# Optimization experiments

Hardware: AMD Instinct MI355X
Metric: run time of the kernel (lower is better)

The kernel has to match this reference:

```python
import jax, jax.numpy as jnp
import numpy as np

T = 32        # time_step
H = 64        # n_hidden (and dense width)
A = 8         # nb_actions
OBS_DIM = 512
B = 4096      # sequences; obs rows = B*T
LN_EPS = 1e-12  # tf.contrib.layers.layer_norm epsilon


def setup_inputs() -> dict:
    key = jax.random.key(0)
    ks = jax.random.split(key, 10)
    s = 0.1
    return {
        "obs":  jax.random.normal(ks[0], (B * T, OBS_DIM), jnp.float32),
        "W0":   jax.random.normal(ks[1], (OBS_DIM, H), jnp.float32) * s,
        "b0":   jnp.zeros((H,), jnp.float32),
        "gamma": jnp.ones((H,), jnp.float32),
        "beta":  jnp.zeros((H,), jnp.float32),
        "Wfw":  jax.random.normal(ks[2], (2 * H, 4 * H), jnp.float32) * s,
        "bfw":  jnp.zeros((4 * H,), jnp.float32),
        "Wbw":  jax.random.normal(ks[3], (2 * H, 4 * H), jnp.float32) * s,
        "bbw":  jnp.zeros((4 * H,), jnp.float32),
        "Wc":   jax.random.uniform(ks[4], (H, A), jnp.float32, -0.003, 0.003),
        "bc":   jnp.zeros((A,), jnp.float32),
    }


def _lstm_scan(xs, W, b):
    """BasicLSTMCell (forget_bias=1.0). xs: [T, B, H] -> hs: [T, B, H]."""
    nb = xs.shape[1]
    init = (jnp.zeros((nb, H), xs.dtype), jnp.zeros((nb, H), xs.dtype))

    def step(carry, x_t):
        c, h = carry
        z = jnp.concatenate([x_t, h], axis=-1) @ W + b  # [B, 4H]
        i, j, f, o = jnp.split(z, 4, axis=-1)           # TF gate order i,j,f,o
        c = c * jax.nn.sigmoid(f + 1.0) + jax.nn.sigmoid(i) * jnp.tanh(j)
        h = jnp.tanh(c) * jax.nn.sigmoid(o)
        return (c, h), h

    _, hs = jax.lax.scan(step, init, xs)
    return hs


def reference(obs, W0, b0, gamma, beta, Wfw, bfw, Wbw, bbw, Wc, bc):
    # dense(64) + layer_norm + relu
    x = obs @ W0 + b0                                   # [B*T, H]
    mu = jnp.mean(x, axis=-1, keepdims=True)
    var = jnp.mean(jnp.square(x - mu), axis=-1, keepdims=True)
    x = gamma * (x - mu) / jnp.sqrt(var + LN_EPS) + beta
    x = jax.nn.relu(x)

    xt = x.reshape(-1, T, H).transpose(1, 0, 2)          # [T, B, H]
    hs_fw = _lstm_scan(xt, Wfw, bfw)                     # [T, B, H]
    hs_bw = _lstm_scan(xt[::-1], Wbw, bbw)[::-1]         # reverse-in, reverse-out

    # tf.reshape on the (fw, bw) tuple stacks along a new leading axis:
    # [2, B, T, H] -> [2B, T*H, 1]; conv1d(kernel=stride=H) == per-step proj.
    y = jnp.stack([hs_fw.transpose(1, 0, 2), hs_bw.transpose(1, 0, 2)], axis=0)
    y = y.reshape(-1, T, H)                              # [2B, T, H]
    out = jnp.tanh(jnp.einsum('btk,ka->bta', y, Wc) + bc)  # [2B, T, A]
    return out
```

## Files before the change

kernel.cpp:

```cpp
#include <hip/hip_runtime.h>
#include <hip/hip_bf16.h>

typedef __attribute__((ext_vector_type(8))) short bf16x8;
typedef __attribute__((ext_vector_type(4))) float f32x4;

#define MFMA_BF16 __builtin_amdgcn_mfma_f32_16x16x32_bf16

#define GLDS16(gp, lp)                                                        \
  __builtin_amdgcn_global_load_lds(                                           \
      (const __attribute__((address_space(1))) void*)(gp),                    \
      (__attribute__((address_space(3))) void*)(lp), 16, 0, 0)

__device__ __forceinline__ unsigned pk2(float a, float b) {
  __hip_bfloat162 t = __float22bfloat162_rn(make_float2(a, b));
  return *reinterpret_cast<unsigned*>(&t);
}
__device__ __forceinline__ unsigned short f2bf_hw(float f) {
  __hip_bfloat16 h = __float2bfloat16(f);
  return *reinterpret_cast<unsigned short*>(&h);
}
__device__ __forceinline__ float tanh_f(float x) {
  return 1.f - 2.f * __builtin_amdgcn_rcpf(1.f + __expf(2.f * x));
}

__global__ void k0_conv(const float* __restrict__ W0, const float* __restrict__ Wfw,
                        const float* __restrict__ Wbw, unsigned short* __restrict__ wfrag,
                        unsigned short* __restrict__ wlstm) {
  int gid = blockIdx.x * 256 + threadIdx.x;
  if (gid < 4096) {
    int f = gid >> 6, l = gid & 63;
    int k0 = (f >> 2) * 32 + ((l >> 4) << 3);
    int n = (f & 3) * 16 + (l & 15);
    bf16x8 v;
#pragma unroll
    for (int j = 0; j < 8; ++j) v[j] = (short)f2bf_hw(W0[(k0 + j) * 64 + n]);
    *(bf16x8*)(wfrag + gid * 8) = v;
  } else if (gid < 12288) {
    int g2 = gid - 4096;
    const float* W = (g2 < 4096) ? Wfw : Wbw;
    int f = (g2 & 4095) >> 6, l = g2 & 63;
    int wv = f >> 4, gate = (f >> 2) & 3, kf = f & 3;
    int col = gate * 64 + wv * 16 + (l & 15);
    int kr = kf * 32 + ((l >> 4) << 3);
    bf16x8 v;
#pragma unroll
    for (int j = 0; j < 8; ++j) v[j] = (short)f2bf_hw(W[(kr + j) * 256 + col]);
    *(bf16x8*)(wlstm + g2 * 8) = v;
  }
}

__global__ __launch_bounds__(256, 3) void k_dense_ln(
    const float* __restrict__ obs, const unsigned short* __restrict__ wfrag,
    const float* __restrict__ b0, const float* __restrict__ gam,
    const float* __restrict__ bet, unsigned short* __restrict__ xout) {
  __shared__ __align__(16) char lds[49152];
  const int tid = threadIdx.x, w = tid >> 6, l = tid & 63;
  const int g = l >> 4, c = l & 15;
  const long blk64 = (long)blockIdx.x * 64;
  const long rb = blk64 + w * 16;

  float b0v[4], gv[4], bv[4];
#pragma unroll
  for (int nt = 0; nt < 4; ++nt) {
    int col = nt * 16 + c;
    b0v[nt] = b0[col]; gv[nt] = gam[col]; bv[nt] = bet[col];
  }
  const unsigned short* wfl = wfrag + l * 8;
  const char* gB = (const char*)obs + blk64 * 2048;

  const int rlo = w * 4 + g;
  asm volatile("s_waitcnt vmcnt(0)" ::: "memory");

#define K1_STAGE(q)                                                           \
  {                                                                           \
    _Pragma("unroll") for (int i = 0; i < 4; ++i) {                           \
      int row_ = i * 16 + rlo;                                                \
      const char* gp_ = gB + (long)row_ * 2048 + (q) * 256 +                  \
                        (long)((c ^ rlo) * 16);                               \
      char* lp_ = lds + ((q) % 3) * 16384 + (i * 4096 + (w * 64 + l) * 16);   \
      GLDS16(gp_, lp_);                                                       \
    }                                                                         \
  }

  K1_STAGE(0);
  K1_STAGE(1);
  K1_STAGE(2);

  f32x4 acc[4];
#pragma unroll
  for (int nt = 0; nt < 4; ++nt) acc[nt] = (f32x4){0.f, 0.f, 0.f, 0.f};

#pragma unroll
  for (int q = 0; q < 8; ++q) {
    constexpr int VW[8] = {8, 16, 24, 24, 24, 24, 20, 16};
    asm volatile("s_waitcnt vmcnt(%0)" :: "i"(VW[q]) : "memory");
    __builtin_amdgcn_s_barrier();
    __builtin_amdgcn_sched_barrier(0);

    const char* rowb = lds + (q % 3) * 16384 + (w * 16 + c) * 256;
#pragma unroll
    for (int kf = 0; kf < 2; ++kf) {
      int fb = (q * 2 + kf) * 4;
      bf16x8 B0 = *(const bf16x8*)(wfl + (fb + 0) * 512);
      bf16x8 B1 = *(const bf16x8*)(wfl + (fb + 1) * 512);
      bf16x8 B2 = *(const bf16x8*)(wfl + (fb + 2) * 512);
      bf16x8 B3 = *(const bf16x8*)(wfl + (fb + 3) * 512);
      int u0 = kf * 8 + g * 2;
      float4 f0 = *(const float4*)(rowb + ((u0 + 0) ^ c) * 16);
      float4 f1 = *(const float4*)(rowb + ((u0 + 1) ^ c) * 16);
      union { bf16x8 v; unsigned u[4]; } af;
      af.u[0] = pk2(f0.x, f0.y); af.u[1] = pk2(f0.z, f0.w);
      af.u[2] = pk2(f1.x, f1.y); af.u[3] = pk2(f1.z, f1.w);
      acc[0] = MFMA_BF16(af.v, B0, acc[0], 0, 0, 0);
      acc[1] = MFMA_BF16(af.v, B1, acc[1], 0, 0, 0);
      acc[2] = MFMA_BF16(af.v, B2, acc[2], 0, 0, 0);
      acc[3] = MFMA_BF16(af.v, B3, acc[3], 0, 0, 0);
    }
    if (q < 5) {
      __builtin_amdgcn_s_barrier();
      __builtin_amdgcn_sched_barrier(0);
      K1_STAGE(q + 3);
    }
  }

  float vv[4][4], s1[4], s2[4];
#pragma unroll
  for (int r = 0; r < 4; ++r) { s1[r] = 0.f; s2[r] = 0.f; }
#pragma unroll
  for (int nt = 0; nt < 4; ++nt)
#pragma unroll
    for (int r = 0; r < 4; ++r) {
      float val = acc[nt][r] + b0v[nt];
      vv[nt][r] = val; s1[r] += val; s2[r] += val * val;
    }
#pragma unroll
  for (int r = 0; r < 4; ++r) {
#pragma unroll
    for (int m = 1; m <= 8; m <<= 1) {
      s1[r] += __shfl_xor(s1[r], m);
      s2[r] += __shfl_xor(s2[r], m);
    }
  }
  unsigned short* xw = (unsigned short*)lds + w * 1024;
#pragma unroll
  for (int r = 0; r < 4; ++r) {
    float mu = s1[r] * 0.015625f;
    float var = s2[r] * 0.015625f - mu * mu;
    float inv = rsqrtf(var + 1e-12f);
    int row = g * 4 + r;
#pragma unroll
    for (int nt = 0; nt < 4; ++nt) {
      float xn = (vv[nt][r] - mu) * inv * gv[nt] + bv[nt];
      xw[(row * 64 + nt * 16 + c) ^ (g << 3)] = f2bf_hw(fmaxf(xn, 0.f));
    }
  }
#pragma unroll
  for (int m2 = 0; m2 < 2; ++m2) {
    int m = m2 * 64 + l;
    int row = m >> 3, u8 = m & 7;
    bf16x8 v = *(const bf16x8*)(xw + ((row * 64 + u8 * 8) ^ ((row >> 2) << 3)));
    *(bf16x8*)(xout + (rb + row) * 64 + u8 * 8) = v;
  }
}

__global__ __launch_bounds__(256, 2) void k_lstm(
    const unsigned short* __restrict__ x, const unsigned short* __restrict__ wlstm,
    const float* __restrict__ bfw, const float* __restrict__ bbw,
    const float* __restrict__ Wc, const float* __restrict__ bc,
    float* __restrict__ out) {
  __shared__ __align__(16) char xr[8 * 2048];
  __shared__ unsigned short hl[2 * 1024];
  __shared__ float pl[16 * 32 * 8];
  const int tid = threadIdx.x, w = tid >> 6, l = tid & 63;
  const int g = l >> 4, c = l & 15;
  const int dir = blockIdx.x >> 8;
  const int sq = (blockIdx.x & 255) * 16;
  const float* bias = dir ? bbw : bfw;

  bf16x8 Bf[4][4];
  const unsigned short* wl = wlstm + ((long)dir * 4096 + w * 16 * 64) * 8;
#pragma unroll
  for (int gate = 0; gate < 4; ++gate)
#pragma unroll
    for (int kf = 0; kf < 4; ++kf)
      Bf[gate][kf] = *(const bf16x8*)(wl + ((gate * 4 + kf) * 64 + l) * 8);
  float bz[4];
#pragma unroll
  for (int gate = 0; gate < 4; ++gate) bz[gate] = bias[gate * 64 + w * 16 + c];

  bf16x8 Pc[2];
#pragma unroll
  for (int kf = 0; kf < 2; ++kf)
#pragma unroll
    for (int j = 0; j < 8; ++j) Pc[kf][j] = 0;
  float bcv = 0.f;
  if (c < 8) {
#pragma unroll
    for (int kf = 0; kf < 2; ++kf)
#pragma unroll
      for (int j = 0; j < 8; ++j)
        Pc[kf][j] = (short)f2bf_hw(Wc[(kf * 32 + g * 8 + j) * 8 + c]);
    bcv = bc[c];
  }

  asm volatile("s_waitcnt vmcnt(0)" ::: "memory");

  const int ss = l >> 3, sc = l & 7;
#define K2_STAGE(tt)                                                          \
  {                                                                           \
    int te_ = dir ? 31 - (tt) : (tt);                                         \
    _Pragma("unroll") for (int p_ = 0; p_ < 2; ++p_) {                        \
      int s_ = p_ * 8 + ss;                                                   \
      const char* gp_ = (const char*)x +                                      \
          ((long)(sq + s_) * 32 + te_) * 128 + (long)(sc ^ (s_ & 7)) * 16;    \
      char* lp_ = xr + ((tt) & 7) * 2048 + p_ * 1024;                         \
      GLDS16(gp_, lp_);                                                       \
    }                                                                         \
  }

  K2_STAGE(w);
  K2_STAGE(w + 4);

  for (int i = tid; i < 1024; i += 256) ((unsigned*)hl)[i] = 0u;
  float cs[4] = {0.f, 0.f, 0.f, 0.f};

  if (w < 2) asm volatile("s_waitcnt vmcnt(2)" ::: "memory");
  asm volatile("s_waitcnt lgkmcnt(0)" ::: "memory");
  __builtin_amdgcn_s_barrier();
  __builtin_amdgcn_sched_barrier(0);

  const int hq = w >> 1;
  const int hgp = ((w & 1) * 2 + (c >> 3)) * 16;
  const int hlo = c & 7;

  f32x4 accx[4];
  {
    const char* xt = xr + c * 128;
    bf16x8 Ax0 = *(const bf16x8*)(xt + (long)((g) ^ (c & 7)) * 16);
    bf16x8 Ax1 = *(const bf16x8*)(xt + (long)((4 + g) ^ (c & 7)) * 16);
#pragma unroll
    for (int gate = 0; gate < 4; ++gate) {
      f32x4 b = (f32x4){bz[gate], bz[gate], bz[gate], bz[gate]};
      accx[gate] = MFMA_BF16(Ax1, Bf[gate][1],
                             MFMA_BF16(Ax0, Bf[gate][0], b, 0, 0, 0), 0, 0, 0);
    }
  }

  int p = 0;
#pragma unroll 2
  for (int t = 0; t < 32; ++t) {
    bf16x8 Ah0 = *(const bf16x8*)((const char*)hl + p * 2048 + l * 16);
    bf16x8 Ah1 = *(const bf16x8*)((const char*)hl + p * 2048 + 1024 + l * 16);

    f32x4 acc[4];
#pragma unroll
    for (int gate = 0; gate < 4; ++gate)
      acc[gate] = MFMA_BF16(Ah1, Bf[gate][3],
                            MFMA_BF16(Ah0, Bf[gate][2], accx[gate], 0, 0, 0),
                            0, 0, 0);

    if (t + 1 < 32) {
      const char* xt = xr + ((t + 1) & 7) * 2048 + c * 128;
      bf16x8 Ax0 = *(const bf16x8*)(xt + (long)((g) ^ (c & 7)) * 16);
      bf16x8 Ax1 = *(const bf16x8*)(xt + (long)((4 + g) ^ (c & 7)) * 16);
#pragma unroll
      for (int gate = 0; gate < 4; ++gate) {
        f32x4 b = (f32x4){bz[gate], bz[gate], bz[gate], bz[gate]};
        accx[gate] = MFMA_BF16(Ax1, Bf[gate][1],
                               MFMA_BF16(Ax0, Bf[gate][0], b, 0, 0, 0), 0, 0, 0);
      }
    }

    const int wb = (p ^ 1) * 1024;
#pragma unroll
    for (int r = 0; r < 4; ++r) {
      float ei = __expf(-acc[0][r]);
      float ej = __expf(2.f * acc[1][r]);
      float ef = __expf(-(acc[2][r] + 1.f));
      float eo = __expf(-acc[3][r]);
      float p12 = (1.f + ei) * (1.f + ej);
      float r3 = __builtin_amdgcn_rcpf(p12 * (1.f + ef));
      float it = (ej - 1.f) * (1.f + ef) * r3;
      float sf = p12 * r3;
      cs[r] = cs[r] * sf + it;
      float ec = __expf(2.f * cs[r]);
      float r2 = __builtin_amdgcn_rcpf((1.f + eo) * (1.f + ec));
      hl[wb + (hq * 64 + hgp + 4 * g + r) * 8 + hlo] = f2bf_hw((ec - 1.f) * r2);
    }

    if (t + 8 < 32 && w == (t & 3)) K2_STAGE(t + 8);

    if (t + 2 < 32 && w == ((t + 2) & 3))
      asm volatile("s_waitcnt vmcnt(2)" ::: "memory");
    asm volatile("s_waitcnt lgkmcnt(0)" ::: "memory");
    __builtin_amdgcn_s_barrier();
    __builtin_amdgcn_sched_barrier(0);

    if (t >= 1) {
      f32x4 pa = (f32x4){0.f, 0.f, 0.f, 0.f};
      pa = MFMA_BF16(Ah0, Pc[0], pa, 0, 0, 0);
      pa = MFMA_BF16(Ah1, Pc[1], pa, 0, 0, 0);
      if (g == w && c < 8) {
        int tp = dir ? 32 - t : t - 1;
#pragma unroll
        for (int r = 0; r < 4; ++r)
          pl[(4 * g + r) * 256 + tp * 8 + c] = tanh_f(pa[r] + bcv);
      }
    }
    p ^= 1;
  }

  {
    bf16x8 Ph0 = *(const bf16x8*)((const char*)hl + p * 2048 + l * 16);
    bf16x8 Ph1 = *(const bf16x8*)((const char*)hl + p * 2048 + 1024 + l * 16);
    f32x4 pa = (f32x4){0.f, 0.f, 0.f, 0.f};
    pa = MFMA_BF16(Ph0, Pc[0], pa, 0, 0, 0);
    pa = MFMA_BF16(Ph1, Pc[1], pa, 0, 0, 0);
    if (g == w && c < 8) {
      int tp = dir ? 0 : 31;
#pragma unroll
      for (int r = 0; r < 4; ++r)
        pl[(4 * g + r) * 256 + tp * 8 + c] = tanh_f(pa[r] + bcv);
    }
  }

  asm volatile("s_waitcnt lgkmcnt(0)" ::: "memory");
  __builtin_amdgcn_s_barrier();
#pragma unroll
  for (int i = 0; i < 4; ++i) {
    int fi = tid + i * 256;
    int s = fi >> 6, rem = fi & 63;
    int t2 = rem >> 1, a4 = (rem & 1) * 4;
    float4 v = *(const float4*)(pl + s * 256 + t2 * 8 + a4);
    *(float4*)(out + ((long)(dir * 4096 + sq + s) * 32 + t2) * 8 + a4) = v;
  }
}

extern "C" void kernel_launch(void* const* d_in, const int* in_sizes, int n_in,
                              void* d_out, int out_size, void* d_ws, size_t ws_size,
                              hipStream_t stream) {
  const float* obs = (const float*)d_in[0];
  const float* W0  = (const float*)d_in[1];
  const float* b0  = (const float*)d_in[2];
  const float* gam = (const float*)d_in[3];
  const float* bet = (const float*)d_in[4];
  const float* Wfw = (const float*)d_in[5];
  const float* bfw = (const float*)d_in[6];
  const float* Wbw = (const float*)d_in[7];
  const float* bbw = (const float*)d_in[8];
  const float* Wc  = (const float*)d_in[9];
  const float* bc  = (const float*)d_in[10];
  float* out = (float*)d_out;

  unsigned short* wfrag = (unsigned short*)d_ws;
  unsigned short* wlstm = wfrag + 4096 * 8;
  unsigned short* xbf   = wlstm + 8192 * 8;

  k0_conv<<<48, 256, 0, stream>>>(W0, Wfw, Wbw, wfrag, wlstm);
  k_dense_ln<<<2048, 256, 0, stream>>>(obs, wfrag, b0, gam, bet, xbf);
  k_lstm<<<512, 256, 0, stream>>>(xbf, wlstm, bfw, bbw, Wc, bc, out);
}
```

Before: 104.1 us.

## Halve sequences per LSTM block to double grid size and parallelism

```diff
diff --git a/kernel.cpp b/kernel.cpp
--- a/kernel.cpp
+++ b/kernel.cpp
@@ -168,13 +168,13 @@
     const float* __restrict__ bfw, const float* __restrict__ bbw,
     const float* __restrict__ Wc, const float* __restrict__ bc,
     float* __restrict__ out) {
-  __shared__ __align__(16) char xr[8 * 2048];
+  __shared__ __align__(16) char xr[8 * 1024];
   __shared__ unsigned short hl[2 * 1024];
-  __shared__ float pl[16 * 32 * 8];
+  __shared__ float pl[8 * 32 * 8];
   const int tid = threadIdx.x, w = tid >> 6, l = tid & 63;
   const int g = l >> 4, c = l & 15;
-  const int dir = blockIdx.x >> 8;
-  const int sq = (blockIdx.x & 255) * 16;
+  const int dir = blockIdx.x >> 9;
+  const int sq = (blockIdx.x & 511) * 8;
   const float* bias = dir ? bbw : bfw;
 
   bf16x8 Bf[4][4];
@@ -209,13 +209,10 @@
 #define K2_STAGE(tt)                                                          \
   {                                                                           \
     int te_ = dir ? 31 - (tt) : (tt);                                         \
-    _Pragma("unroll") for (int p_ = 0; p_ < 2; ++p_) {                        \
-      int s_ = p_ * 8 + ss;                                                   \
-      const char* gp_ = (const char*)x +                                      \
-          ((long)(sq + s_) * 32 + te_) * 128 + (long)(sc ^ (s_ & 7)) * 16;    \
-      char* lp_ = xr + ((tt) & 7) * 2048 + p_ * 1024;                         \
-      GLDS16(gp_, lp_);                                                       \
-    }                                                                         \
+    const char* gp_ = (const char*)x +                                        \
+        ((long)(sq + ss) * 32 + te_) * 128 + (long)((sc ^ ss) * 16);          \
+    char* lp_ = xr + ((tt) & 7) * 1024;                                       \
+    GLDS16(gp_, lp_);                                                         \
   }
 
   K2_STAGE(w);
@@ -224,20 +221,20 @@
   for (int i = tid; i < 1024; i += 256) ((unsigned*)hl)[i] = 0u;
   float cs[4] = {0.f, 0.f, 0.f, 0.f};
 
-  if (w < 2) asm volatile("s_waitcnt vmcnt(2)" ::: "memory");
+  if (w < 2) asm volatile("s_waitcnt vmcnt(1)" ::: "memory");
   asm volatile("s_waitcnt lgkmcnt(0)" ::: "memory");
   __builtin_amdgcn_s_barrier();
   __builtin_amdgcn_sched_barrier(0);
 
-  const int hq = w >> 1;
-  const int hgp = ((w & 1) * 2 + (c >> 3)) * 16;
-  const int hlo = c & 7;
+  const int hf = w >> 1;
+  const int hlb = 16 * ((w * 2 + (c >> 3)) & 3);
+  const int hj = c & 7;
 
   f32x4 accx[4];
   {
-    const char* xt = xr + c * 128;
-    bf16x8 Ax0 = *(const bf16x8*)(xt + (long)((g) ^ (c & 7)) * 16);
-    bf16x8 Ax1 = *(const bf16x8*)(xt + (long)((4 + g) ^ (c & 7)) * 16);
+    const char* xt = xr + (c & 7) * 128;
+    bf16x8 Ax0 = *(const bf16x8*)(xt + (long)((g ^ (c & 7)) * 16));
+    bf16x8 Ax1 = *(const bf16x8*)(xt + (long)(((4 + g) ^ (c & 7)) * 16));
 #pragma unroll
     for (int gate = 0; gate < 4; ++gate) {
       f32x4 b = (f32x4){bz[gate], bz[gate], bz[gate], bz[gate]};
@@ -260,9 +257,9 @@
                             0, 0, 0);
 
     if (t + 1 < 32) {
-      const char* xt = xr + ((t + 1) & 7) * 2048 + c * 128;
-      bf16x8 Ax0 = *(const bf16x8*)(xt + (long)((g) ^ (c & 7)) * 16);
-      bf16x8 Ax1 = *(const bf16x8*)(xt + (long)((4 + g) ^ (c & 7)) * 16);
+      const char* xt = xr + ((t + 1) & 7) * 1024 + (c & 7) * 128;
+      bf16x8 Ax0 = *(const bf16x8*)(xt + (long)((g ^ (c & 7)) * 16));
+      bf16x8 Ax1 = *(const bf16x8*)(xt + (long)(((4 + g) ^ (c & 7)) * 16));
 #pragma unroll
       for (int gate = 0; gate < 4; ++gate) {
         f32x4 b = (f32x4){bz[gate], bz[gate], bz[gate], bz[gate]};
@@ -272,35 +269,37 @@
     }
 
     const int wb = (p ^ 1) * 1024;
-#pragma unroll
-    for (int r = 0; r < 4; ++r) {
-      float ei = __expf(-acc[0][r]);
-      float ej = __expf(2.f * acc[1][r]);
-      float ef = __expf(-(acc[2][r] + 1.f));
-      float eo = __expf(-acc[3][r]);
-      float p12 = (1.f + ei) * (1.f + ej);
-      float r3 = __builtin_amdgcn_rcpf(p12 * (1.f + ef));
-      float it = (ej - 1.f) * (1.f + ef) * r3;
-      float sf = p12 * r3;
-      cs[r] = cs[r] * sf + it;
-      float ec = __expf(2.f * cs[r]);
-      float r2 = __builtin_amdgcn_rcpf((1.f + eo) * (1.f + ec));
-      hl[wb + (hq * 64 + hgp + 4 * g + r) * 8 + hlo] = f2bf_hw((ec - 1.f) * r2);
-    }
-
-    if (t + 8 < 32 && w == (t & 3)) K2_STAGE(t + 8);
+    if (g < 2) {
+#pragma unroll
+      for (int r = 0; r < 4; ++r) {
+        float ei = __expf(-acc[0][r]);
+        float ej = __expf(2.f * acc[1][r]);
+        float ef = __expf(-(acc[2][r] + 1.f));
+        float eo = __expf(-acc[3][r]);
+        float p12 = (1.f + ei) * (1.f + ej);
+        float r3 = __builtin_amdgcn_rcpf(p12 * (1.f + ef));
+        float it = (ej - 1.f) * (1.f + ef) * r3;
+        float sf = p12 * r3;
+        cs[r] = cs[r] * sf + it;
+        float ec = __expf(2.f * cs[r]);
+        float r2 = __builtin_amdgcn_rcpf((1.f + eo) * (1.f + ec));
+        hl[wb + hf * 512 + (hlb + 4 * g + r) * 8 + hj] = f2bf_hw((ec - 1.f) * r2);
+      }
+    }
 
     if (t + 2 < 32 && w == ((t + 2) & 3))
-      asm volatile("s_waitcnt vmcnt(2)" ::: "memory");
+      asm volatile("s_waitcnt vmcnt(1)" ::: "memory");
     asm volatile("s_waitcnt lgkmcnt(0)" ::: "memory");
     __builtin_amdgcn_s_barrier();
     __builtin_amdgcn_sched_barrier(0);
+
+    if (t + 8 < 32 && w == (t & 3)) K2_STAGE(t + 8);
 
     if (t >= 1) {
       f32x4 pa = (f32x4){0.f, 0.f, 0.f, 0.f};
       pa = MFMA_BF16(Ah0, Pc[0], pa, 0, 0, 0);
       pa = MFMA_BF16(Ah1, Pc[1], pa, 0, 0, 0);
-      if (g == w && c < 8) {
+      if (w < 2 && g == w && c < 8) {
         int tp = dir ? 32 - t : t - 1;
 #pragma unroll
         for (int r = 0; r < 4; ++r)
@@ -316,7 +315,7 @@
     f32x4 pa = (f32x4){0.f, 0.f, 0.f, 0.f};
     pa = MFMA_BF16(Ph0, Pc[0], pa, 0, 0, 0);
     pa = MFMA_BF16(Ph1, Pc[1], pa, 0, 0, 0);
-    if (g == w && c < 8) {
+    if (w < 2 && g == w && c < 8) {
       int tp = dir ? 0 : 31;
 #pragma unroll
       for (int r = 0; r < 4; ++r)
@@ -327,7 +326,7 @@
   asm volatile("s_waitcnt lgkmcnt(0)" ::: "memory");
   __builtin_amdgcn_s_barrier();
 #pragma unroll
-  for (int i = 0; i < 4; ++i) {
+  for (int i = 0; i < 2; ++i) {
     int fi = tid + i * 256;
     int s = fi >> 6, rem = fi & 63;
     int t2 = rem >> 1, a4 = (rem & 1) * 4;
@@ -358,5 +357,5 @@
 
   k0_conv<<<48, 256, 0, stream>>>(W0, Wfw, Wbw, wfrag, wlstm);
   k_dense_ln<<<2048, 256, 0, stream>>>(obs, wfrag, b0, gam, bet, xbf);
-  k_lstm<<<512, 256, 0, stream>>>(xbf, wlstm, bfw, bbw, Wc, bc, out);
-}
+  k_lstm<<<1024, 256, 0, stream>>>(xbf, wlstm, bfw, bbw, Wc, bc, out);
+}
```

Result: slower. 127.6 us (+22.5%).

## Replace LDS-staged obs pipeline with direct register prefetch in dense+LN kernel

Applied to the files above, without the earlier changes.

```diff
diff --git a/kernel.cpp b/kernel.cpp
--- a/kernel.cpp
+++ b/kernel.cpp
@@ -53,11 +53,10 @@
     const float* __restrict__ obs, const unsigned short* __restrict__ wfrag,
     const float* __restrict__ b0, const float* __restrict__ gam,
     const float* __restrict__ bet, unsigned short* __restrict__ xout) {
-  __shared__ __align__(16) char lds[49152];
+  __shared__ unsigned short xs[4096];
   const int tid = threadIdx.x, w = tid >> 6, l = tid & 63;
   const int g = l >> 4, c = l & 15;
-  const long blk64 = (long)blockIdx.x * 64;
-  const long rb = blk64 + w * 16;
+  const long rb = (long)blockIdx.x * 64 + w * 16;
 
   float b0v[4], gv[4], bv[4];
 #pragma unroll
@@ -65,61 +64,49 @@
     int col = nt * 16 + c;
     b0v[nt] = b0[col]; gv[nt] = gam[col]; bv[nt] = bet[col];
   }
+
+  const float* arow = obs + (rb + c) * 512 + g * 8;
   const unsigned short* wfl = wfrag + l * 8;
-  const char* gB = (const char*)obs + blk64 * 2048;
-
-  const int rlo = w * 4 + g;
-  asm volatile("s_waitcnt vmcnt(0)" ::: "memory");
-
-#define K1_STAGE(q)                                                           \
-  {                                                                           \
-    _Pragma("unroll") for (int i = 0; i < 4; ++i) {                           \
-      int row_ = i * 16 + rlo;                                                \
-      const char* gp_ = gB + (long)row_ * 2048 + (q) * 256 +                  \
-                        (long)((c ^ rlo) * 16);                               \
-      char* lp_ = lds + ((q) % 3) * 16384 + (i * 4096 + (w * 64 + l) * 16);   \
-      GLDS16(gp_, lp_);                                                       \
-    }                                                                         \
-  }
-
-  K1_STAGE(0);
-  K1_STAGE(1);
-  K1_STAGE(2);
+
+  float4 pa[4], pb[4];
+#pragma unroll
+  for (int d = 0; d < 4; ++d) {
+    pa[d] = *(const float4*)(arow + d * 32);
+    pb[d] = *(const float4*)(arow + d * 32 + 4);
+  }
+  bf16x8 Bc[4];
+#pragma unroll
+  for (int nt = 0; nt < 4; ++nt) Bc[nt] = *(const bf16x8*)(wfl + nt * 512);
 
   f32x4 acc[4];
 #pragma unroll
   for (int nt = 0; nt < 4; ++nt) acc[nt] = (f32x4){0.f, 0.f, 0.f, 0.f};
 
 #pragma unroll
-  for (int q = 0; q < 8; ++q) {
-    constexpr int VW[8] = {8, 16, 24, 24, 24, 24, 20, 16};
-    asm volatile("s_waitcnt vmcnt(%0)" :: "i"(VW[q]) : "memory");
-    __builtin_amdgcn_s_barrier();
-    __builtin_amdgcn_sched_barrier(0);
-
-    const char* rowb = lds + (q % 3) * 16384 + (w * 16 + c) * 256;
-#pragma unroll
-    for (int kf = 0; kf < 2; ++kf) {
-      int fb = (q * 2 + kf) * 4;
-      bf16x8 B0 = *(const bf16x8*)(wfl + (fb + 0) * 512);
-      bf16x8 B1 = *(const bf16x8*)(wfl + (fb + 1) * 512);
-      bf16x8 B2 = *(const bf16x8*)(wfl + (fb + 2) * 512);
-      bf16x8 B3 = *(const bf16x8*)(wfl + (fb + 3) * 512);
-      int u0 = kf * 8 + g * 2;
-      float4 f0 = *(const float4*)(rowb + ((u0 + 0) ^ c) * 16);
-      float4 f1 = *(const float4*)(rowb + ((u0 + 1) ^ c) * 16);
-      union { bf16x8 v; unsigned u[4]; } af;
-      af.u[0] = pk2(f0.x, f0.y); af.u[1] = pk2(f0.z, f0.w);
-      af.u[2] = pk2(f1.x, f1.y); af.u[3] = pk2(f1.z, f1.w);
-      acc[0] = MFMA_BF16(af.v, B0, acc[0], 0, 0, 0);
-      acc[1] = MFMA_BF16(af.v, B1, acc[1], 0, 0, 0);
-      acc[2] = MFMA_BF16(af.v, B2, acc[2], 0, 0, 0);
-      acc[3] = MFMA_BF16(af.v, B3, acc[3], 0, 0, 0);
-    }
-    if (q < 5) {
-      __builtin_amdgcn_s_barrier();
-      __builtin_amdgcn_sched_barrier(0);
-      K1_STAGE(q + 3);
+  for (int kf = 0; kf < 16; ++kf) {
+    const int slot = kf & 3;
+    union { bf16x8 v; unsigned u[4]; } af;
+    af.u[0] = pk2(pa[slot].x, pa[slot].y);
+    af.u[1] = pk2(pa[slot].z, pa[slot].w);
+    af.u[2] = pk2(pb[slot].x, pb[slot].y);
+    af.u[3] = pk2(pb[slot].z, pb[slot].w);
+    if (kf + 4 < 16) {
+      pa[slot] = *(const float4*)(arow + (kf + 4) * 32);
+      pb[slot] = *(const float4*)(arow + (kf + 4) * 32 + 4);
+    }
+    bf16x8 Bn[4];
+    if (kf < 15) {
+#pragma unroll
+      for (int nt = 0; nt < 4; ++nt)
+        Bn[nt] = *(const bf16x8*)(wfl + ((kf + 1) * 4 + nt) * 512);
+    }
+    acc[0] = MFMA_BF16(af.v, Bc[0], acc[0], 0, 0, 0);
+    acc[1] = MFMA_BF16(af.v, Bc[1], acc[1], 0, 0, 0);
+    acc[2] = MFMA_BF16(af.v, Bc[2], acc[2], 0, 0, 0);
+    acc[3] = MFMA_BF16(af.v, Bc[3], acc[3], 0, 0, 0);
+    if (kf < 15) {
+#pragma unroll
+      for (int nt = 0; nt < 4; ++nt) Bc[nt] = Bn[nt];
     }
   }
 
@@ -141,7 +128,7 @@
       s2[r] += __shfl_xor(s2[r], m);
     }
   }
-  unsigned short* xw = (unsigned short*)lds + w * 1024;
+  unsigned short* xw = xs + w * 1024;
 #pragma unroll
   for (int r = 0; r < 4; ++r) {
     float mu = s1[r] * 0.015625f;
```

Result: slower. 113.7 us (+9.2%).
